# Kernel tuning notes

Measured on AMD Instinct MI355X. Metric: run time of the kernel, lower is better.

The kernel has to match this reference:

```python
import jax, jax.numpy as jnp
import numpy as np

B, S, D = 1, 2048, 2048
H, KV, HD = 16, 2, 128        # heads, kv heads, head_dim
Q_SIZE, KV_SIZE = H * HD, KV * HD
NEG = -1e9


def setup_inputs() -> dict:
    key = jax.random.key(0)
    ks = jax.random.split(key, 5)
    hidden_states = jax.random.normal(ks[0], (B, S, D), dtype=jnp.float32)
    # rotary tables (Gemma/Qwen style: theta=10000, half-dim frequencies)
    inv_freq = 1.0 / (10000.0 ** (jnp.arange(0, HD, 2, dtype=jnp.float32) / HD))  # [HD/2]
    angles = jnp.arange(S, dtype=jnp.float32)[:, None] * inv_freq[None, :]        # [S, HD/2]
    freqs_cos = jnp.cos(angles)
    freqs_sin = jnp.sin(angles)
    kv_write_indices = jnp.arange(S, dtype=jnp.int32)
    k_cache = jnp.zeros((B, S, KV, HD), dtype=jnp.float32)
    v_cache = jnp.zeros((B, S, KV, HD), dtype=jnp.float32)
    causal = jnp.tril(jnp.ones((S, S), dtype=bool))
    mask = jnp.where(causal, 0.0, NEG).astype(jnp.float32)[None, None]  # [1,1,S,S]
    W_qkv = jax.random.normal(ks[1], (D, Q_SIZE + 2 * KV_SIZE), dtype=jnp.float32) * (D ** -0.5)
    b_qkv = jax.random.normal(ks[2], (Q_SIZE + 2 * KV_SIZE,), dtype=jnp.float32) * 0.02
    W_o = jax.random.normal(ks[3], (Q_SIZE, D), dtype=jnp.float32) * (Q_SIZE ** -0.5)
    return {
        "hidden_states": hidden_states, "freqs_cos": freqs_cos, "freqs_sin": freqs_sin,
        "kv_write_indices": kv_write_indices, "k_cache": k_cache, "v_cache": v_cache,
        "mask": mask, "W_qkv": W_qkv, "b_qkv": b_qkv, "W_o": W_o,
    }


def _rope(x, cos, sin):
    # x: [B, S, h, HD]; cos/sin: [S, HD/2]. Half-split (Gemma complex) layout.
    x1, x2 = jnp.split(x, 2, axis=-1)
    c = cos[None, :, None, :]
    s = sin[None, :, None, :]
    return jnp.concatenate([x1 * c - x2 * s, x1 * s + x2 * c], axis=-1)


def reference(hidden_states, freqs_cos, freqs_sin, kv_write_indices,
              k_cache, v_cache, mask, W_qkv, b_qkv, W_o):
    b, s, _ = hidden_states.shape
    qkv = hidden_states @ W_qkv + b_qkv                       # [B,S,(H+2KV)*HD]
    xq, xk, xv = jnp.split(qkv, [Q_SIZE, Q_SIZE + KV_SIZE], axis=-1)
    xq = xq.reshape(b, s, H, HD)
    xk = xk.reshape(b, s, KV, HD)
    xv = xv.reshape(b, s, KV, HD)
    xq = _rope(xq, freqs_cos, freqs_sin)
    xk = _rope(xk, freqs_cos, freqs_sin)
    # KV-cache write (index_copy_ along seq dim)
    key = k_cache.at[:, kv_write_indices].set(xk)             # [B,T,KV,HD]
    value = v_cache.at[:, kv_write_indices].set(xv)
    # GQA: repeat_interleave kv heads to H
    nrep = H // KV
    key = jnp.repeat(key, nrep, axis=2)                       # [B,T,H,HD]
    value = jnp.repeat(value, nrep, axis=2)
    q = jnp.transpose(xq, (0, 2, 1, 3)) * (HD ** -0.5)        # [B,H,S,HD]
    k = jnp.transpose(key, (0, 2, 1, 3))                      # [B,H,T,HD]
    v = jnp.transpose(value, (0, 2, 1, 3))
    scores = jnp.einsum("bhqd,bhkd->bhqk", q, k) + mask       # [B,H,S,T]
    probs = jax.nn.softmax(scores, axis=-1)
    out = jnp.einsum("bhqk,bhkd->bhqd", probs, v)             # [B,H,S,HD]
    out = jnp.transpose(out, (0, 2, 1, 3)).reshape(b, s, Q_SIZE)
    return out @ W_o                                          # [B,S,D]
```

## Files before the change

### kernel.cpp

```cpp
#include <hip/hip_runtime.h>
#include <hip/hip_bf16.h>

#define S_LEN 2048
#define D_MODEL 2048
#define NH 16
#define NKV 2
#define HD 128
#define QKV_N 2560
#define Q_SCALE_L2E (0.08838834764831845f * 1.4426950408889634f)

typedef short short8 __attribute__((ext_vector_type(8)));
typedef short s16x4 __attribute__((ext_vector_type(4)));
typedef float f32x4 __attribute__((ext_vector_type(4)));
using u16 = unsigned short;

__device__ inline u16 f2b(float x) {
  __hip_bfloat16 h = __float2bfloat16(x);
  return *(u16*)&h;
}
__device__ inline float b2f(u16 x) {
  __hip_bfloat16 h = *(__hip_bfloat16*)&x;
  return __bfloat162float(h);
}
__device__ inline bool is_f32(const unsigned int* fc) {
  return (fc[0] & 0xFFFFu) == 0u;
}
__device__ inline u16 ld_cvt(const void* p, size_t i, bool f32) {
  return f32 ? f2b(((const float*)p)[i]) : ((const u16*)p)[i];
}

__device__ inline void async_copy16(const u16* g, u16* l) {
  __builtin_amdgcn_global_load_lds(
      (const __attribute__((address_space(1))) unsigned int*)g,
      (__attribute__((address_space(3))) unsigned int*)l, 16, 0, 0);
}

__global__ void convert_k(const void* __restrict__ in, u16* __restrict__ out,
                          int n, const unsigned int* __restrict__ fc) {
  const bool f32 = is_f32(fc);
  int i = blockIdx.x * 256 + threadIdx.x;
  if (i < n) out[i] = ld_cvt(in, i, f32);
}

__global__ void prep_k(const void* __restrict__ fcos, const void* __restrict__ fsin,
                       const void* __restrict__ bqkv, u16* __restrict__ cCos,
                       u16* __restrict__ cSin, u16* __restrict__ cBias) {
  const bool f32 = is_f32((const unsigned int*)fcos);
  int i = blockIdx.x * 256 + threadIdx.x;
  if (i < 131072)       cCos[i] = ld_cvt(fcos, i, f32);
  else if (i < 262144)  cSin[i - 131072] = ld_cvt(fsin, i - 131072, f32);
  else if (i < 264704)  cBias[i - 262144] = ld_cvt(bqkv, i - 262144, f32);
}

__global__ void transpose_k(const void* __restrict__ in, u16* __restrict__ out,
                            int R, int C, const unsigned int* __restrict__ fc) {
  __shared__ u16 tile[64][65];
  const bool f32 = is_f32(fc);
  const int t = threadIdx.x;
  const int r0 = blockIdx.y * 64, c0 = blockIdx.x * 64;
  for (int i = 0; i < 16; ++i) {
    int idx = i * 256 + t;
    int r = idx >> 6, c = idx & 63;
    tile[r][c] = ld_cvt(in, (size_t)(r0 + r) * C + c0 + c, f32);
  }
  __syncthreads();
  for (int i = 0; i < 16; ++i) {
    int idx = i * 256 + t;
    int r = idx >> 6, c = idx & 63;
    out[(size_t)(c0 + r) * R + r0 + c] = tile[c][r];
  }
}

template<int M, int N, int K, int KS>
__global__ __launch_bounds__(256, 2) void gemm_splitk(const u16* __restrict__ A,
                                                      const u16* __restrict__ BT,
                                                      u16* __restrict__ P0,
                                                      u16* __restrict__ P1) {
  __shared__ __align__(16) u16 lA[16 * 64 * 8];
  __shared__ __align__(16) u16 lB[16 * 64 * 8];
  const int t = threadIdx.x, lane = t & 63, w = t >> 6;
  const int wr = w & 1, wc = w >> 1;
  const int m0 = blockIdx.y * 128, n0 = blockIdx.x * 128;
  const int koff = blockIdx.z * KS;
  const int l15 = lane & 15, quad = lane >> 4;
  const int swz = (quad * 16 + (l15 ^ quad)) * 8;

  int srcoff[4], sdst[4];
  for (int qq = 0; qq < 4; ++qq) {
    int f = qq * 256 + t;
    int row = f >> 3, kc = f & 7;
    int j = kc >> 2, q4 = kc & 3, tile = row >> 4, lr = row & 15;
    sdst[qq] = ((j * 8 + tile) * 64 + q4 * 16 + (lr ^ q4)) * 8;
    srcoff[qq] = row * K + kc * 8;
  }

  f32x4 acc[4][4] = {};
  for (int k0 = koff; k0 < koff + KS; k0 += 64) {
    short8 av[4], bv[4];
    for (int qq = 0; qq < 4; ++qq) {
      av[qq] = *(const short8*)&A [(size_t)m0 * K + k0 + srcoff[qq]];
      bv[qq] = *(const short8*)&BT[(size_t)n0 * K + k0 + srcoff[qq]];
    }
    __syncthreads();
    for (int qq = 0; qq < 4; ++qq) {
      *(short8*)&lA[sdst[qq]] = av[qq];
      *(short8*)&lB[sdst[qq]] = bv[qq];
    }
    __syncthreads();
    for (int j = 0; j < 2; ++j) {
      short8 af[4], bf[4];
      for (int i = 0; i < 4; ++i)
        af[i] = *(const short8*)&lA[(j * 8 + wr * 4 + i) * 512 + swz];
      for (int jj = 0; jj < 4; ++jj)
        bf[jj] = *(const short8*)&lB[(j * 8 + wc * 4 + jj) * 512 + swz];
      for (int i = 0; i < 4; ++i)
        for (int jj = 0; jj < 4; ++jj)
          acc[i][jj] = __builtin_amdgcn_mfma_f32_16x16x32_bf16(af[i], bf[jj],
                                                               acc[i][jj], 0, 0, 0);
    }
  }

  u16* P = blockIdx.z ? P1 : P0;
  for (int i = 0; i < 4; ++i)
    for (int jj = 0; jj < 4; ++jj) {
      int row = m0 + wr * 64 + i * 16 + quad * 4;
      int col = n0 + wc * 64 + jj * 16 + l15;
      for (int r = 0; r < 4; ++r)
        P[(size_t)(row + r) * N + col] = f2b(acc[i][jj][r]);
    }
}


__global__ void rope_k(const u16* __restrict__ P0, const u16* __restrict__ P1,
                       const u16* __restrict__ bias, const u16* __restrict__ cosT,
                       const u16* __restrict__ sinT, const int* __restrict__ idx,
                       u16* __restrict__ q, u16* __restrict__ kfrag) {
  const int s = blockIdx.y;
  const int c = blockIdx.x * 256 + threadIdx.x;
  const bool isq = c < 2048;
  int d, colbase;
  if (isq) { d = c & 127; colbase = c & ~127; }
  else     { int c2 = c - 2048; d = c2 & 127; colbase = 2048 + (c2 & ~127); }
  const int dd = d & 63;
  const size_t b1 = (size_t)s * QKV_N + colbase + dd;
  float x1 = b2f(P0[b1]) + b2f(P1[b1]) + b2f(bias[colbase + dd]);
  float x2 = b2f(P0[b1 + 64]) + b2f(P1[b1 + 64]) + b2f(bias[colbase + dd + 64]);
  float cv = b2f(cosT[s * 64 + dd]);
  float sv = b2f(sinT[s * 64 + dd]);
  float v = (d < 64) ? (x1 * cv - x2 * sv) : (x1 * sv + x2 * cv);
  if (isq) {
    q[(size_t)s * D_MODEL + c] = f2b(v * Q_SCALE_L2E);
  } else {
    int c2 = c - 2048;
    int kvh = c2 >> 7, dcol = c2 & 127;
    int srow = idx[s];
    int sblk = srow >> 6, ns = (srow >> 4) & 3, lr = srow & 15;
    int cc = dcol >> 5, qd = (dcol >> 3) & 3, j = dcol & 7;
    kfrag[kvh * 262144 + sblk * 8192 + ((ns * 4 + cc) * 64 + qd * 16 + lr) * 8 + j] = f2b(v);
  }
}

__global__ void vscat_k(const u16* __restrict__ P0, const u16* __restrict__ P1,
                        const u16* __restrict__ bias, const int* __restrict__ idx,
                        u16* __restrict__ vfrag) {
  int id = blockIdx.x * 256 + threadIdx.x;
  int s = id >> 8, cv = id & 255;
  int kvh = cv >> 7, dcol = cv & 127;
  const size_t gi = (size_t)s * QKV_N + 2304 + cv;
  float v = b2f(P0[gi]) + b2f(P1[gi]) + b2f(bias[2304 + cv]);
  int srow = idx[s];
  int sblk = srow >> 6, kvl = srow & 63;
  int c2 = kvl >> 5, qd = (kvl >> 2) & 3, j = ((kvl >> 4) & 1) * 4 + (kvl & 3);
  int d = dcol >> 4, lr = dcol & 15;
  vfrag[kvh * 262144 + sblk * 8192 + ((c2 * 8 + d) * 64 + qd * 16 + lr) * 8 + j] = f2b(v);
}

__global__ void reduce_out_k(const u16* __restrict__ G0, const u16* __restrict__ G1,
                             void* __restrict__ out, const unsigned int* __restrict__ fc) {
  const bool f32 = is_f32(fc);
  int i = blockIdx.x * 256 + threadIdx.x;
  float v = b2f(G0[i]) + b2f(G1[i]);
  if (f32) ((float*)out)[i] = v;
  else     ((u16*)out)[i] = f2b(v);
}

__global__ __launch_bounds__(256, 3) void attn_part_k(const u16* __restrict__ Q,
                                                      const u16* __restrict__ Kf,
                                                      const u16* __restrict__ Vf,
                                                      u16* __restrict__ attnOut,
                                                      u16* __restrict__ pO_A,
                                                      u16* __restrict__ pO_B,
                                                      float* __restrict__ ml) {
  __shared__ __align__(16) u16 sm[16384];
  const int t = threadIdx.x, lane = t & 63, w = t >> 6;
  const int l15 = lane & 15, quad = lane >> 4;

  const int b = blockIdx.x;
  const int plane = b / 160;
  const int u = 159 - (b - plane * 160);
  int g, rp, c;
  if (u < 16)      { g = 0; rp = u;                   c = 0; }
  else if (u < 48) { int z = u - 16; g = 1; rp = 16 + (z >> 1); c = z & 1; }
  else if (u < 96) { int z = u - 48; g = 2; rp = 32 + z / 3;    c = z % 3; }
  else             { int z = u - 96; g = 3; rp = 48 + (z >> 2); c = z & 3; }
  const int kvh = plane >> 1, hh = plane & 1;
  const int h = kvh * 8 + hh * 4 + w;
  const int qrow0 = rp * 32;
  const int kv_lo = c * 512;
  const int kv_hi = min(kv_lo + 512, qrow0 + 32);
  const int nkb = (kv_hi - kv_lo + 63) >> 6;
  const bool direct = (g == 0);
  const int gw = b * 4 + w;

  const u16* Kb = Kf + kvh * 262144;
  const u16* Vb = Vf + kvh * 262144;

  short8 aq[2][4];
  for (int ss = 0; ss < 2; ++ss)
    for (int cc = 0; cc < 4; ++cc)
      aq[ss][cc] = *(const short8*)&Q[(size_t)(qrow0 + ss * 16 + l15) * D_MODEL
                                      + h * HD + cc * 32 + quad * 8];

  f32x4 oacc[2][8] = {};
  float m_i[2] = {-1e30f, -1e30f}, l_i[2] = {0.0f, 0.0f};

  {
    const u16* kt = Kb + (size_t)(kv_lo >> 6) * 8192;
    const u16* vt = Vb + (size_t)(kv_lo >> 6) * 8192;
    for (int f = 0; f < 4; ++f) {
      int fr = w * 4 + f;
      async_copy16(kt + fr * 512 + lane * 8, &sm[fr * 512]);
      async_copy16(vt + fr * 512 + lane * 8, &sm[8192 + fr * 512]);
    }
  }
  __syncthreads();

  for (int kb = 0; kb < nkb; ++kb) {
    const int kv0 = kv_lo + kb * 64;
    f32x4 st[2][4] = {};
    for (int ns = 0; ns < 4; ++ns) {
      short8 bk[4];
      for (int cc = 0; cc < 4; ++cc)
        bk[cc] = *(const short8*)&sm[((ns * 4 + cc) * 64 + lane) * 8];
      for (int ss = 0; ss < 2; ++ss)
        for (int cc = 0; cc < 4; ++cc)
          st[ss][ns] = __builtin_amdgcn_mfma_f32_16x16x32_bf16(bk[cc], aq[ss][cc],
                                                               st[ss][ns], 0, 0, 0);
    }
    __syncthreads();
    if (kb + 1 < nkb) {
      const u16* kt = Kb + (size_t)((kv0 + 64) >> 6) * 8192;
      for (int f = 0; f < 4; ++f) {
        int fr = w * 4 + f;
        async_copy16(kt + fr * 512 + lane * 8, &sm[fr * 512]);
      }
    }
    const bool need_mask = (kv0 + 63) > qrow0;
    short8 pb[2][2];
    for (int ss = 0; ss < 2; ++ss) {
      float mb = -1e30f;
      if (need_mask) {
        int qg = qrow0 + ss * 16 + l15;
        #pragma unroll
        for (int ns = 0; ns < 4; ++ns) {
          int kvg = kv0 + ns * 16 + quad * 4;
          #pragma unroll
          for (int rr = 0; rr < 4; ++rr) {
            float s = (kvg + rr <= qg) ? st[ss][ns][rr] : -1e30f;
            st[ss][ns][rr] = s;
            mb = fmaxf(mb, s);
          }
        }
      } else {
        #pragma unroll
        for (int ns = 0; ns < 4; ++ns)
          #pragma unroll
          for (int rr = 0; rr < 4; ++rr) mb = fmaxf(mb, st[ss][ns][rr]);
      }
      mb = fmaxf(mb, __shfl_xor(mb, 16, 64));
      mb = fmaxf(mb, __shfl_xor(mb, 32, 64));
      if (!__all(mb <= m_i[ss] + 8.0f)) {
        float mn = fmaxf(m_i[ss], mb);
        float alpha = exp2f(m_i[ss] - mn);
        m_i[ss] = mn;
        l_i[ss] *= alpha;
        #pragma unroll
        for (int dt = 0; dt < 8; ++dt) oacc[ss][dt] *= alpha;
      }
      float rs = 0.0f;
      #pragma unroll
      for (int ns = 0; ns < 4; ++ns)
        #pragma unroll
        for (int rr = 0; rr < 4; ++rr) {
          float e = exp2f(st[ss][ns][rr] - m_i[ss]);
          rs += e;
          pb[ss][ns >> 1][(ns & 1) * 4 + rr] = (short)f2b(e);
        }
      rs += __shfl_xor(rs, 16, 64);
      rs += __shfl_xor(rs, 32, 64);
      l_i[ss] += rs;
    }
    for (int c2 = 0; c2 < 2; ++c2)
      for (int dt = 0; dt < 8; ++dt) {
        short8 av = *(const short8*)&sm[8192 + ((c2 * 8 + dt) * 64 + lane) * 8];
        for (int ss = 0; ss < 2; ++ss)
          oacc[ss][dt] = __builtin_amdgcn_mfma_f32_16x16x32_bf16(av, pb[ss][c2],
                                                                 oacc[ss][dt], 0, 0, 0);
      }
    if (kb + 1 < nkb) {
      __syncthreads();
      const u16* vt = Vb + (size_t)((kv0 + 64) >> 6) * 8192;
      for (int f = 0; f < 4; ++f) {
        int fr = w * 4 + f;
        async_copy16(vt + fr * 512 + lane * 8, &sm[8192 + fr * 512]);
      }
    }
  }

  __syncthreads();
  u16* Ow = &sm[w * 2176];
  const int er = lane >> 2, ec = lane & 3;
  for (int ss = 0; ss < 2; ++ss) {
    float inv = direct ? (1.0f / l_i[ss]) : 1.0f;
    for (int dt = 0; dt < 8; ++dt) {
      s16x4 pk;
      for (int rr = 0; rr < 4; ++rr) pk[rr] = (short)f2b(oacc[ss][dt][rr] * inv);
      *(s16x4*)&Ow[l15 * 136 + dt * 16 + quad * 4] = pk;
    }
    __builtin_amdgcn_s_waitcnt(0xC07F);
    short8 o0 = *(const short8*)&Ow[er * 136 + ec * 32];
    short8 o1 = *(const short8*)&Ow[er * 136 + ec * 32 + 8];
    short8 o2 = *(const short8*)&Ow[er * 136 + ec * 32 + 16];
    short8 o3 = *(const short8*)&Ow[er * 136 + ec * 32 + 24];
    __builtin_amdgcn_s_waitcnt(0xC07F);
    if (direct) {
      size_t ga = (size_t)(qrow0 + ss * 16 + er) * D_MODEL + h * HD + ec * 32;
      *(short8*)&attnOut[ga]      = o0;
      *(short8*)&attnOut[ga + 8]  = o1;
      *(short8*)&attnOut[ga + 16] = o2;
      *(short8*)&attnOut[ga + 24] = o3;
    } else {
      u16* po = (gw < 2048) ? (pO_A + (size_t)gw * 4096)
                            : (pO_B + (size_t)(gw - 2048) * 4096);
      int ra = (ss * 16 + er) * 128 + ec * 32;
      *(short8*)&po[ra]      = o0;
      *(short8*)&po[ra + 8]  = o1;
      *(short8*)&po[ra + 16] = o2;
      *(short8*)&po[ra + 24] = o3;
      if (quad == 0) {
        ml[gw * 64 + (ss * 16 + l15) * 2]     = m_i[ss];
        ml[gw * 64 + (ss * 16 + l15) * 2 + 1] = l_i[ss];
      }
    }
  }
}

__global__ void attn_combine_k(const u16* __restrict__ pO_A,
                               const u16* __restrict__ pO_B,
                               const float* __restrict__ ml,
                               u16* __restrict__ attn) {
  const int cbk = blockIdx.x;
  const int h = cbk / 48, rp = 16 + (cbk - (cbk / 48) * 48);
  const int g = rp >> 4, nch = g + 1;
  const int t = threadIdx.x;
  const int row = t >> 3;
  const int dblk = t & 7;
  const int plane = (h >> 3) * 2 + ((h >> 2) & 1);
  const int w = h & 3;
  static const int baseg[4] = {0, 16, 48, 96};

  int gws[4];
  float wt[4];
  float mx = -1e30f;
  for (int c = 0; c < nch; ++c) {
    int u = baseg[g] + (rp - (g << 4)) * nch + c;
    int b = plane * 160 + (159 - u);
    gws[c] = b * 4 + w;
    mx = fmaxf(mx, ml[gws[c] * 64 + row * 2]);
  }
  float lsum = 0.0f;
  for (int c = 0; c < nch; ++c) {
    float m = ml[gws[c] * 64 + row * 2];
    float l = ml[gws[c] * 64 + row * 2 + 1];
    wt[c] = exp2f(m - mx);
    lsum += l * wt[c];
  }
  float inv = 1.0f / lsum;
  const size_t orow = (size_t)(rp * 32 + row) * D_MODEL + h * HD + dblk * 16;
  for (int j = 0; j < 16; ++j) {
    float acc = 0.0f;
    for (int c = 0; c < nch; ++c) {
      const u16* po = (gws[c] < 2048) ? (pO_A + (size_t)gws[c] * 4096)
                                      : (pO_B + (size_t)(gws[c] - 2048) * 4096);
      acc += b2f(po[row * 128 + dblk * 16 + j]) * wt[c];
    }
    attn[orow + j] = f2b(acc * inv);
  }
}

extern "C" void kernel_launch(void* const* d_in, const int* in_sizes, int n_in,
                              void* d_out, int out_size, void* d_ws, size_t ws_size,
                              hipStream_t stream) {
  const void* hidden = d_in[0];
  const void* fcos   = d_in[1];
  const void* fsin   = d_in[2];
  const int* idx     = (const int*)d_in[3];
  u16* maskScratch   = (u16*)d_in[6];
  const void* Wqkv = d_in[7];
  const void* bqkv = d_in[8];
  const void* Wo   = d_in[9];
  const unsigned int* fc = (const unsigned int*)fcos;

  u16* ws = (u16*)d_ws;
  u16* cHid   = ws;
  u16* cCos   = ws + 4194304;
  u16* cSin   = ws + 4325376;
  u16* cBias  = ws + 4456448;
  u16* WqkvT  = ws + 4461056;
  u16* q      = WqkvT;
  u16* G1     = WqkvT;
  u16* P0     = ws + 9703936;
  u16* attn   = P0;
  u16* P1     = ws + 14946816;
  u16* pO_B   = P1;
  float* ml   = (float*)(P1 + 2097152);
  u16* WoT    = ws + 20189696;
  u16* kfrag  = ws;
  u16* vfrag  = ws + 524288;
  u16* G0     = ws;

  convert_k<<<(4194304 + 255) / 256, 256, 0, stream>>>(hidden, cHid, 4194304, fc);
  prep_k<<<(264704 + 255) / 256, 256, 0, stream>>>(fcos, fsin, bqkv, cCos, cSin, cBias);
  transpose_k<<<dim3(40, 32), 256, 0, stream>>>(Wqkv, WqkvT, D_MODEL, QKV_N, fc);
  transpose_k<<<dim3(32, 32), 256, 0, stream>>>(Wo, WoT, D_MODEL, D_MODEL, fc);
  gemm_splitk<S_LEN, QKV_N, D_MODEL, D_MODEL / 2>
      <<<dim3(QKV_N / 128, S_LEN / 128, 2), 256, 0, stream>>>(cHid, WqkvT, P0, P1);
  rope_k<<<dim3(9, S_LEN), 256, 0, stream>>>(P0, P1, cBias, cCos, cSin, idx, q, kfrag);
  vscat_k<<<2048, 256, 0, stream>>>(P0, P1, cBias, idx, vfrag);
  attn_part_k<<<640, 256, 0, stream>>>(q, kfrag, vfrag, attn, maskScratch, pO_B, ml);
  attn_combine_k<<<16 * 48, 256, 0, stream>>>(maskScratch, pO_B, ml, attn);
  gemm_splitk<S_LEN, D_MODEL, D_MODEL, D_MODEL / 2>
      <<<dim3(D_MODEL / 128, S_LEN / 128, 2), 256, 0, stream>>>(attn, WoT, G0, G1);
  reduce_out_k<<<4194304 / 256, 256, 0, stream>>>(G0, G1, d_out, fc);
}
```

Measured before the change: 279.3 us.

## Balance attention KV-split work with a greedy partition table and MFMA priority hints

```diff
diff --git a/kernel.cpp b/kernel.cpp
--- a/kernel.cpp
+++ b/kernel.cpp
@@ -9,6 +9,8 @@
 #define QKV_N 2560
 #define Q_SCALE_L2E (0.08838834764831845f * 1.4426950408889634f)
 
+#define EPP 192
+
 typedef short short8 __attribute__((ext_vector_type(8)));
 typedef short s16x4 __attribute__((ext_vector_type(4)));
 typedef float f32x4 __attribute__((ext_vector_type(4)));
@@ -33,6 +35,45 @@
   __builtin_amdgcn_global_load_lds(
       (const __attribute__((address_space(1))) unsigned int*)g,
       (__attribute__((address_space(3))) unsigned int*)l, 16, 0, 0);
+}
+
+__global__ void mkpart_k(int* __restrict__ tab) {
+  if (threadIdx.x != 0) return;
+  int T[64], n[64];
+  int S = 0;
+  for (int rp = 0; rp < 64; ++rp) {
+    T[rp] = (rp + 2) >> 1;
+    n[rp] = (T[rp] + 5) / 6;
+    S += n[rp];
+  }
+  while (S > EPP) {
+    int best = -1, bc = 1 << 30;
+    for (int rp = 0; rp < 64; ++rp)
+      if (n[rp] > 1) {
+        int c = (T[rp] + n[rp] - 2) / (n[rp] - 1);
+        if (c < bc) { bc = c; best = rp; }
+      }
+    --n[best]; --S;
+  }
+  while (S < EPP) {
+    int best = -1, bc = -1;
+    for (int rp = 0; rp < 64; ++rp)
+      if (n[rp] < T[rp]) {
+        int c = (T[rp] + n[rp] - 1) / n[rp];
+        if (c > bc) { bc = c; best = rp; }
+      }
+    ++n[best]; ++S;
+  }
+  int e = 0;
+  for (int rp = 0; rp < 64; ++rp) {
+    tab[EPP + rp] = e;
+    tab[EPP + 64 + rp] = n[rp];
+    for (int c = 0; c < n[rp]; ++c) {
+      int tlo = c * T[rp] / n[rp];
+      int thi = (c + 1) * T[rp] / n[rp];
+      tab[e++] = rp | (tlo << 6) | ((thi - tlo) << 12) | ((n[rp] == 1) ? (1 << 18) : 0);
+    }
+  }
 }
 
 __global__ void convert_k(const void* __restrict__ in, u16* __restrict__ out,
@@ -187,6 +228,7 @@
 __global__ __launch_bounds__(256, 3) void attn_part_k(const u16* __restrict__ Q,
                                                       const u16* __restrict__ Kf,
                                                       const u16* __restrict__ Vf,
+                                                      const int* __restrict__ tab,
                                                       u16* __restrict__ attnOut,
                                                       u16* __restrict__ pO_A,
                                                       u16* __restrict__ pO_B,
@@ -196,20 +238,14 @@
   const int l15 = lane & 15, quad = lane >> 4;
 
   const int b = blockIdx.x;
-  const int plane = b / 160;
-  const int u = 159 - (b - plane * 160);
-  int g, rp, c;
-  if (u < 16)      { g = 0; rp = u;                   c = 0; }
-  else if (u < 48) { int z = u - 16; g = 1; rp = 16 + (z >> 1); c = z & 1; }
-  else if (u < 96) { int z = u - 48; g = 2; rp = 32 + z / 3;    c = z % 3; }
-  else             { int z = u - 96; g = 3; rp = 48 + (z >> 2); c = z & 3; }
+  const int plane = b / EPP;
+  const int ent = tab[b - plane * EPP];
+  const int rp = ent & 63, tlo = (ent >> 6) & 63, nkb = (ent >> 12) & 63;
+  const bool direct = (ent >> 18) & 1;
   const int kvh = plane >> 1, hh = plane & 1;
   const int h = kvh * 8 + hh * 4 + w;
   const int qrow0 = rp * 32;
-  const int kv_lo = c * 512;
-  const int kv_hi = min(kv_lo + 512, qrow0 + 32);
-  const int nkb = (kv_hi - kv_lo + 63) >> 6;
-  const bool direct = (g == 0);
+  const int kv_lo = tlo * 64;
   const int gw = b * 4 + w;
 
   const u16* Kb = Kf + kvh * 262144;
@@ -238,6 +274,7 @@
   for (int kb = 0; kb < nkb; ++kb) {
     const int kv0 = kv_lo + kb * 64;
     f32x4 st[2][4] = {};
+    __builtin_amdgcn_s_setprio(1);
     for (int ns = 0; ns < 4; ++ns) {
       short8 bk[4];
       for (int cc = 0; cc < 4; ++cc)
@@ -247,6 +284,7 @@
           st[ss][ns] = __builtin_amdgcn_mfma_f32_16x16x32_bf16(bk[cc], aq[ss][cc],
                                                                st[ss][ns], 0, 0, 0);
     }
+    __builtin_amdgcn_s_setprio(0);
     __syncthreads();
     if (kb + 1 < nkb) {
       const u16* kt = Kb + (size_t)((kv0 + 64) >> 6) * 8192;
@@ -300,6 +338,7 @@
       rs += __shfl_xor(rs, 32, 64);
       l_i[ss] += rs;
     }
+    __builtin_amdgcn_s_setprio(1);
     for (int c2 = 0; c2 < 2; ++c2)
       for (int dt = 0; dt < 8; ++dt) {
         short8 av = *(const short8*)&sm[8192 + ((c2 * 8 + dt) * 64 + lane) * 8];
@@ -307,6 +346,7 @@
           oacc[ss][dt] = __builtin_amdgcn_mfma_f32_16x16x32_bf16(av, pb[ss][c2],
                                                                  oacc[ss][dt], 0, 0, 0);
       }
+    __builtin_amdgcn_s_setprio(0);
     if (kb + 1 < nkb) {
       __syncthreads();
       const u16* vt = Vb + (size_t)((kv0 + 64) >> 6) * 8192;
@@ -358,24 +398,23 @@
 __global__ void attn_combine_k(const u16* __restrict__ pO_A,
                                const u16* __restrict__ pO_B,
                                const float* __restrict__ ml,
+                               const int* __restrict__ tab,
                                u16* __restrict__ attn) {
-  const int cbk = blockIdx.x;
-  const int h = cbk / 48, rp = 16 + (cbk - (cbk / 48) * 48);
-  const int g = rp >> 4, nch = g + 1;
+  const int h = blockIdx.x >> 6, rp = blockIdx.x & 63;
+  const int nch = tab[EPP + 64 + rp];
+  if (nch == 1) return;
+  const int start = tab[EPP + rp];
   const int t = threadIdx.x;
   const int row = t >> 3;
   const int dblk = t & 7;
   const int plane = (h >> 3) * 2 + ((h >> 2) & 1);
   const int w = h & 3;
-  static const int baseg[4] = {0, 16, 48, 96};
-
-  int gws[4];
-  float wt[4];
+
+  int gws[8];
+  float wt[8];
   float mx = -1e30f;
   for (int c = 0; c < nch; ++c) {
-    int u = baseg[g] + (rp - (g << 4)) * nch + c;
-    int b = plane * 160 + (159 - u);
-    gws[c] = b * 4 + w;
+    gws[c] = (plane * EPP + start + c) * 4 + w;
     mx = fmaxf(mx, ml[gws[c] * 64 + row * 2]);
   }
   float lsum = 0.0f;
@@ -416,6 +455,7 @@
   u16* cCos   = ws + 4194304;
   u16* cSin   = ws + 4325376;
   u16* cBias  = ws + 4456448;
+  int* tab    = (int*)(ws + 4459008);
   u16* WqkvT  = ws + 4461056;
   u16* q      = WqkvT;
   u16* G1     = WqkvT;
@@ -423,12 +463,13 @@
   u16* attn   = P0;
   u16* P1     = ws + 14946816;
   u16* pO_B   = P1;
-  float* ml   = (float*)(P1 + 2097152);
+  float* ml   = (float*)(P1 + 4194304);
   u16* WoT    = ws + 20189696;
   u16* kfrag  = ws;
   u16* vfrag  = ws + 524288;
   u16* G0     = ws;
 
+  mkpart_k<<<1, 64, 0, stream>>>(tab);
   convert_k<<<(4194304 + 255) / 256, 256, 0, stream>>>(hidden, cHid, 4194304, fc);
   prep_k<<<(264704 + 255) / 256, 256, 0, stream>>>(fcos, fsin, bqkv, cCos, cSin, cBias);
   transpose_k<<<dim3(40, 32), 256, 0, stream>>>(Wqkv, WqkvT, D_MODEL, QKV_N, fc);
@@ -437,8 +478,8 @@
       <<<dim3(QKV_N / 128, S_LEN / 128, 2), 256, 0, stream>>>(cHid, WqkvT, P0, P1);
   rope_k<<<dim3(9, S_LEN), 256, 0, stream>>>(P0, P1, cBias, cCos, cSin, idx, q, kfrag);
   vscat_k<<<2048, 256, 0, stream>>>(P0, P1, cBias, idx, vfrag);
-  attn_part_k<<<640, 256, 0, stream>>>(q, kfrag, vfrag, attn, maskScratch, pO_B, ml);
-  attn_combine_k<<<16 * 48, 256, 0, stream>>>(maskScratch, pO_B, ml, attn);
+  attn_part_k<<<4 * EPP, 256, 0, stream>>>(q, kfrag, vfrag, tab, attn, maskScratch, pO_B, ml);
+  attn_combine_k<<<16 * 64, 256, 0, stream>>>(maskScratch, pO_B, ml, tab, attn);
   gemm_splitk<S_LEN, D_MODEL, D_MODEL, D_MODEL / 2>
       <<<dim3(D_MODEL / 128, S_LEN / 128, 2), 256, 0, stream>>>(attn, WoT, G0, G1);
   reduce_out_k<<<4194304 / 256, 256, 0, stream>>>(G0, G1, d_out, fc);
```

Result: slower. 483.6 us (+73.1%).
